# Optimization experiments

Hardware: AMD Instinct MI355X
Metric: run time of the kernel (lower is better)

## Reference

```python
import jax, jax.numpy as jnp
import numpy as np

M0, M1 = 16, 8          # scalar / vector multiplicities (16x0e + 8x1o)
NB = 16                  # number_of_basis
RMAX = 8.0               # max_radius
N_NODES, N_EDGES = 10000, 160000
WNUM = M0*M0 + M0*M1 + M1*M1 + M1*M0  # 576, tp weight_numel


def sus(t):
    """e3nn soft_unit_step: exp(-1/t) for t>0 else 0."""
    safe = jnp.where(t > 0, t, 1.0)
    return jnp.where(t > 0, jnp.exp(-1.0 / safe), 0.0)


def setup_inputs():
    key = jax.random.key(0)
    ks = jax.random.split(key, 12)
    D = M0 + 3 * M1  # 40
    x = jax.random.normal(ks[0], (N_NODES, D), jnp.float32)
    edge_index = jax.random.randint(ks[1], (2, N_EDGES), 0, N_NODES, jnp.int32)
    edge_attr = jax.random.normal(ks[2], (N_EDGES, 4), jnp.float32)  # sh lmax=1
    node_attr = jnp.ones((N_NODES, 1), jnp.float32)
    batch = jnp.zeros((N_NODES,), jnp.int32)
    amf = jax.random.uniform(ks[3], (N_EDGES, 1), jnp.float32) * RMAX  # edge lengths
    Wq0 = jax.random.normal(ks[4], (M0, M0), jnp.float32)
    Wq1 = jax.random.normal(ks[5], (M1, M1), jnp.float32)
    Wk1 = jax.random.normal(ks[6], (NB, 16), jnp.float32)
    Wk2 = jax.random.normal(ks[7], (16, WNUM), jnp.float32)
    Wv1 = jax.random.normal(ks[8], (NB, 16), jnp.float32)
    Wv2 = jax.random.normal(ks[9], (16, WNUM), jnp.float32)
    Wd0 = jax.random.normal(ks[10], (M0, M0), jnp.float32)
    Wd1 = jax.random.normal(ks[11], (M1, M1), jnp.float32)
    return dict(x=x, edge_index=edge_index, edge_attr=edge_attr, node_attr=node_attr,
                batch=batch, additional_message_features=amf,
                Wq0=Wq0, Wq1=Wq1, Wk1=Wk1, Wk2=Wk2, Wv1=Wv1, Wv2=Wv2, Wd0=Wd0, Wd1=Wd1)


def reference(x, edge_index, edge_attr, node_attr, batch, additional_message_features,
              Wq0, Wq1, Wk1, Wk2, Wv1, Wv2, Wd0, Wd1):
    n = x.shape[0]
    src, dst = edge_index[0], edge_index[1]
    d = additional_message_features.reshape(-1)  # [E]

    # soft_one_hot_linspace(basis='smooth_finite', cutoff=True) * sqrt(NB)
    centers = jnp.linspace(0.0, RMAX, NB + 2)[1:-1]
    step = RMAX / (NB + 1)
    diff = (d[:, None] - centers) / step
    emb = (1.14136 * np.exp(2.0)) * sus(diff + 1.0) * sus(1.0 - diff) * np.sqrt(NB)  # [E,NB]
    cutoff = sus(10.0 * (1.0 - d / RMAX))  # [E]

    # split irreps: scalars [*,M0], vectors [*,M1,3]
    x0 = x[:, :M0]
    x1 = x[:, M0:].reshape(n, M1, 3)

    # q = Linear(input_irreps -> hidden_irreps): per-irrep linear, 1/sqrt(fan_in)
    q0 = (x0 @ Wq0) / np.sqrt(M0)
    q1 = jnp.einsum('nui,uw->nwi', x1, Wq1) / np.sqrt(M1)

    # radial MLPs producing per-edge tensor-product weights
    def radial(W1, W2):
        h = jax.nn.silu((emb @ W1) / np.sqrt(NB))
        return (h @ W2) / np.sqrt(16.0)  # [E, WNUM]
    wk = radial(Wk1, Wk2)
    wv = radial(Wv1, Wv2)

    xs0, xs1 = x0[src], x1[src]           # gather by edge source
    sh0, sh1 = edge_attr[:, 0], edge_attr[:, 1:4]
    dot11 = jnp.einsum('eui,ei->eu', xs1, sh1) / np.sqrt(3.0)  # 1o x 1o -> 0e CG

    def fctp(w):
        # FullyConnectedTensorProduct(input, sh, out) with per-edge weights.
        s1 = M0 * M0
        s2 = s1 + M0 * M1
        s3 = s2 + M1 * M1
        w1 = w[:, :s1].reshape(-1, M0, M0)   # 0e x 0e -> 0e
        w2 = w[:, s1:s2].reshape(-1, M0, M1) # 0e x 1o -> 1o
        w3 = w[:, s2:s3].reshape(-1, M1, M1) # 1o x 0e -> 1o
        w4 = w[:, s3:].reshape(-1, M1, M0)   # 1o x 1o -> 0e
        norm = 1.0 / np.sqrt(M0 + M1)        # path fan-in normalization
        o0 = (jnp.einsum('euw,eu->ew', w1, xs0 * sh0[:, None]) +
              jnp.einsum('euw,eu->ew', w4, dot11)) * norm            # [E,M0]
        o1 = (jnp.einsum('euw,eu,ei->ewi', w2, xs0, sh1) +
              jnp.einsum('euw,eui->ewi', w3, xs1 * sh0[:, None, None])) * norm  # [E,M1,3]
        return o0, o1

    k0, k1 = fctp(wk)
    v0, v1 = fctp(wv)

    # dot: FullyConnectedTensorProduct(hidden, hidden, '0e') with shared weights
    score = (jnp.einsum('eu,ev,uv->e', q0[dst], k0, Wd0) +
             jnp.einsum('eui,evi,uv->e', q1[dst], k1, Wd1) / np.sqrt(3.0)) / np.sqrt(M0*M0 + M1*M1)

    expv = cutoff * jnp.exp(score)                                   # [E]
    z = jax.ops.segment_sum(expv, dst, num_segments=n)               # [N]
    z = jnp.where(z == 0, 1.0, z)
    alpha = expv / z[dst]
    we = jnp.sqrt(jax.nn.relu(alpha))                                # alpha.relu().sqrt()
    v = jnp.concatenate([v0, v1.reshape(-1, 3 * M1)], axis=1)        # [E,40]
    return jax.ops.segment_sum(we[:, None] * v, dst, num_segments=n) # [N,40]
```

## Files before the change

### kernel.cpp

```cpp
#include <hip/hip_runtime.h>
#include <hip/hip_bf16.h>

#define E_CNT 160000
#define N_CNT 10000

#define INV_STEP   2.125f
#define EMB_C      33.734292f
#define INVS320    0.05590170f
#define INVS8      0.35355339f
#define INV_SQRT3  0.57735027f
#define KSCALE     0.051031036f

#define OFF_FLAG   0
#define OFF_XF     16
#define OFF_EAF    400016
#define OFF_AMFF   1040016
#define OFF_WQ0F   1200016
#define OFF_WQ1F   1200272
#define OFF_WD0F   1200336
#define OFF_WD1F   1200592
#define OFF_WK1F   1200656
#define OFF_WV1F   1200912
#define OFF_WK2F   1201168
#define OFF_WV2F   1210384
#define OFF_P      1219600
#define OFF_EXPV   1619600
#define OFF_VBUF   1779600
#define OFF_DEG    8179600
#define OFF_Z      8179600
#define OFF_DEG2   8189600
#define OFF_START  8199600
#define OFF_START2 8209601
#define OFF_CURS   8219602
#define OFF_CURS2  8229602
#define OFF_DPOS   8239602
#define OFF_ELIST2 8399602
#define OFF_G      8559632

static __device__ __forceinline__ float bf2f(__hip_bfloat16 b) { return __bfloat162float(b); }
static __device__ __forceinline__ float sanitize(float v) {
    return fminf(fmaxf(v, -1e30f), 1e30f);
}
static __device__ __forceinline__ unsigned short f2bf(float f) {
    unsigned x = __float_as_uint(f);
    unsigned r = (x + 0x7fffu + ((x >> 16) & 1u)) >> 16;
    return (unsigned short)r;
}
static __device__ __forceinline__ float bflo(unsigned u) { return __uint_as_float(u << 16); }
static __device__ __forceinline__ float bfhi(unsigned u) { return __uint_as_float(u & 0xffff0000u); }

static __device__ __forceinline__ float4 load4(const void* p, int i4, int f32)
{
    if (f32) return ((const float4*)p)[i4];
    uint2 u = ((const uint2*)p)[i4];
    float4 r;
    r.x = bflo(u.x); r.y = bfhi(u.x);
    r.z = bflo(u.y); r.w = bfhi(u.y);
    return r;
}

__global__ __launch_bounds__(256) void prep_kernel(
    const void* __restrict__ x,   const void* __restrict__ ea,  const void* __restrict__ amf,
    const void* __restrict__ Wq0, const void* __restrict__ Wq1,
    const void* __restrict__ Wk1, const void* __restrict__ Wk2,
    const void* __restrict__ Wv1, const void* __restrict__ Wv2,
    const void* __restrict__ Wd0, const void* __restrict__ Wd1,
    const int* __restrict__ ei, float* __restrict__ ws)
{
    __shared__ int sflag;
    const int tid = threadIdx.x;
    if (tid == 0) {
        const unsigned short* xb = (const unsigned short*)x;
        int cnt = 0;
        for (int k = 0; k < 256; k += 2) {
            unsigned e = (unsigned)((xb[k] >> 7) & 0xFF);
            if (e >= 141) ++cnt;
        }
        sflag = (cnt >= 8) ? 1 : 0;
        if (blockIdx.x == 0) *(int*)ws = sflag;
    }
    __syncthreads();
    const int f32 = sflag;
    const int i = blockIdx.x * 256 + tid;

    if (i < 100000) ((float4*)(ws + OFF_XF))[i] = load4(x, i, f32);
    if (i < 160000) ((float4*)(ws + OFF_EAF))[i] = load4(ea, i, f32);
    if (i < 40000)  ((float4*)(ws + OFF_AMFF))[i] = load4(amf, i, f32);
    if (i < 40000) {
#pragma unroll
        for (int k = 0; k < 4; ++k) {
            atomicAdd((int*)(ws + OFF_DEG)  + ei[E_CNT + 4 * i + k], 1);
            atomicAdd((int*)(ws + OFF_DEG2) + ei[4 * i + k], 1);
        }
    }
    if (i < 2304) {
        ((float4*)(ws + OFF_WK2F))[i] = load4(Wk2, i, f32);
        ((float4*)(ws + OFF_WV2F))[i] = load4(Wv2, i, f32);
    }
    if (i < 64) {
        ((float4*)(ws + OFF_WQ0F))[i] = load4(Wq0, i, f32);
        ((float4*)(ws + OFF_WD0F))[i] = load4(Wd0, i, f32);
        ((float4*)(ws + OFF_WK1F))[i] = load4(Wk1, i, f32);
        ((float4*)(ws + OFF_WV1F))[i] = load4(Wv1, i, f32);
    }
    if (i < 16) {
        ((float4*)(ws + OFF_WQ1F))[i] = load4(Wq1, i, f32);
        ((float4*)(ws + OFF_WD1F))[i] = load4(Wd1, i, f32);
    }
}

__global__ __launch_bounds__(512) void scan_kernel(float* __restrict__ ws)
{
    __shared__ int ssum[512];
    const int t    = threadIdx.x;
    const int half = t >> 8;
    const int lt   = t & 255;
    int* deg   = (int*)(ws + (half ? OFF_DEG2   : OFF_DEG));
    int* start = (int*)(ws + (half ? OFF_START2 : OFF_START));
    int* curs  = (int*)(ws + (half ? OFF_CURS2  : OFF_CURS));
    const int base = lt * 40;
    int s = 0;
    for (int k = 0; k < 40; ++k) {
        int idx = base + k;
        if (idx < N_CNT) s += deg[idx];
    }
    ssum[t] = s;
    __syncthreads();
    for (int off = 1; off < 256; off <<= 1) {
        int v = (lt >= off) ? ssum[t - off] : 0;
        __syncthreads();
        ssum[t] += v;
        __syncthreads();
    }
    int run = ssum[t] - s;
    for (int k = 0; k < 40; ++k) {
        int idx = base + k;
        if (idx < N_CNT) {
            start[idx] = run;
            curs[idx]  = run;
            run += deg[idx];
        }
    }
    if (lt == 255) start[N_CNT] = E_CNT;
    __syncthreads();
    for (int k = t; k < N_CNT; k += 512) ws[OFF_Z + k] = 0.f;
}

__global__ __launch_bounds__(256) void fillgp_kernel(const int* __restrict__ ei, float* __restrict__ ws)
{
    const int blk = blockIdx.x;
    const int tid = threadIdx.x;
    if (blk < 625) {
        const int e = blk * 256 + tid;
        int pd = atomicAdd((int*)(ws + OFF_CURS)  + ei[E_CNT + e], 1);
        int ps = atomicAdd((int*)(ws + OFF_CURS2) + ei[e], 1);
        ((int*)(ws + OFF_ELIST2))[ps] = e;
        ((int*)(ws + OFF_DPOS))[ps]   = pd;
        return;
    }
    if (blk >= 1875) {
        const int n = (blk - 1875) * 256 + tid;
        if (n >= N_CNT) return;
        const float* WQ0 = ws + OFF_WQ0F;
        const float* WQ1 = ws + OFF_WQ1F;
        const float* WD0 = ws + OFF_WD0F;
        const float* WD1 = ws + OFF_WD1F;
        float xs[40];
        const float4* xr = (const float4*)(ws + OFF_XF + n * 40);
#pragma unroll
        for (int k = 0; k < 10; ++k) {
            float4 f = xr[k];
            xs[4 * k + 0] = f.x; xs[4 * k + 1] = f.y; xs[4 * k + 2] = f.z; xs[4 * k + 3] = f.w;
        }
        float q0[16];
#pragma unroll
        for (int w = 0; w < 16; ++w) {
            float s = 0.f;
#pragma unroll
            for (int u = 0; u < 16; ++u) s = fmaf(xs[u], WQ0[u * 16 + w], s);
            q0[w] = s * 0.25f;
        }
        float* pn = ws + OFF_P + n * 40;
#pragma unroll
        for (int v = 0; v < 16; ++v) {
            float s = 0.f;
#pragma unroll
            for (int w = 0; w < 16; ++w) s = fmaf(q0[w], WD0[w * 16 + v], s);
            pn[v] = sanitize(s * INVS320);
        }
        float q1[24];
#pragma unroll
        for (int w = 0; w < 8; ++w) {
            float s0 = 0.f, s1 = 0.f, s2 = 0.f;
#pragma unroll
            for (int u = 0; u < 8; ++u) {
                float wq = WQ1[u * 8 + w];
                s0 = fmaf(xs[16 + u * 3 + 0], wq, s0);
                s1 = fmaf(xs[16 + u * 3 + 1], wq, s1);
                s2 = fmaf(xs[16 + u * 3 + 2], wq, s2);
            }
            q1[w * 3 + 0] = s0 * INVS8;
            q1[w * 3 + 1] = s1 * INVS8;
            q1[w * 3 + 2] = s2 * INVS8;
        }
#pragma unroll
        for (int v = 0; v < 8; ++v) {
            float s0 = 0.f, s1 = 0.f, s2 = 0.f;
#pragma unroll
            for (int w = 0; w < 8; ++w) {
                float wd = WD1[w * 8 + v];
                s0 = fmaf(q1[w * 3 + 0], wd, s0);
                s1 = fmaf(q1[w * 3 + 1], wd, s1);
                s2 = fmaf(q1[w * 3 + 2], wd, s2);
            }
            const float sc = INVS320 * INV_SQRT3;
            pn[16 + v * 3 + 0] = sanitize(s0 * sc);
            pn[16 + v * 3 + 1] = sanitize(s1 * sc);
            pn[16 + v * 3 + 2] = sanitize(s2 * sc);
        }
        return;
    }
    const int t = (blk - 625) * 256 + tid;
    const int p   = t / 160000;
    const int rem = t - p * 160000;
    const int c   = rem / 10000;
    const int n   = rem - c * 10000;

    const float* W2 = ws + (p ? OFF_WV2F : OFF_WK2F) + c * 576;
    float x0[16], x1[24];
    {
        const float4* xr = (const float4*)(ws + OFF_XF + n * 40);
        float xs[40];
#pragma unroll
        for (int k = 0; k < 10; ++k) {
            float4 f = xr[k];
            xs[4 * k + 0] = f.x; xs[4 * k + 1] = f.y; xs[4 * k + 2] = f.z; xs[4 * k + 3] = f.w;
        }
#pragma unroll
        for (int u = 0; u < 16; ++u) x0[u] = xs[u];
#pragma unroll
        for (int u = 0; u < 24; ++u) x1[u] = xs[16 + u];
    }

    float out[96];
#pragma unroll
    for (int w = 0; w < 16; ++w) {
        float s = 0.f;
#pragma unroll
        for (int u = 0; u < 16; ++u) s = fmaf(W2[u * 16 + w], x0[u], s);
        out[w] = s;
    }
#pragma unroll
    for (int w = 0; w < 8; ++w) {
        float s = 0.f;
#pragma unroll
        for (int u = 0; u < 16; ++u) s = fmaf(W2[256 + u * 8 + w], x0[u], s);
        out[16 + w] = s;
    }
#pragma unroll
    for (int w = 0; w < 8; ++w) {
        float s0 = 0.f, s1 = 0.f, s2 = 0.f;
#pragma unroll
        for (int u = 0; u < 8; ++u) {
            float wv = W2[384 + u * 8 + w];
            s0 = fmaf(wv, x1[u * 3 + 0], s0);
            s1 = fmaf(wv, x1[u * 3 + 1], s1);
            s2 = fmaf(wv, x1[u * 3 + 2], s2);
        }
        out[24 + w * 3 + 0] = s0;
        out[24 + w * 3 + 1] = s1;
        out[24 + w * 3 + 2] = s2;
    }
#pragma unroll
    for (int w = 0; w < 16; ++w) {
        float s0 = 0.f, s1 = 0.f, s2 = 0.f;
#pragma unroll
        for (int u = 0; u < 8; ++u) {
            float wv = W2[448 + u * 16 + w];
            s0 = fmaf(wv, x1[u * 3 + 0], s0);
            s1 = fmaf(wv, x1[u * 3 + 1], s1);
            s2 = fmaf(wv, x1[u * 3 + 2], s2);
        }
        out[48 + w * 3 + 0] = s0 * INV_SQRT3;
        out[48 + w * 3 + 1] = s1 * INV_SQRT3;
        out[48 + w * 3 + 2] = s2 * INV_SQRT3;
    }

    uint4 ov[12];
    unsigned* ou = (unsigned*)ov;
#pragma unroll
    for (int k = 0; k < 48; ++k)
        ou[k] = (unsigned)f2bf(out[2 * k]) | ((unsigned)f2bf(out[2 * k + 1]) << 16);
    uint4* dp = (uint4*)((unsigned short*)(ws + OFF_G) + ((size_t)n * 2 + p) * 1536 + c * 96);
#pragma unroll
    for (int q = 0; q < 12; ++q) dp[q] = ov[q];
}

static __device__ __forceinline__ void load48(unsigned (&ub)[48], const uint4* __restrict__ rp)
{
#pragma unroll
    for (int q = 0; q < 12; ++q) {
        uint4 v = rp[q];
        ub[4 * q + 0] = v.x; ub[4 * q + 1] = v.y;
        ub[4 * q + 2] = v.z; ub[4 * q + 3] = v.w;
    }
}

static __device__ __forceinline__ void accum48(const unsigned (&ub)[48], float hc, float sh0,
    float s1x, float s1y, float s1z,
    float (&o0)[16], float (&o1)[24], float (&t2a)[8])
{
    const float hs = hc * sh0;
#define GVAL(k) (((k) & 1) ? bfhi(ub[(k) >> 1]) : bflo(ub[(k) >> 1]))
#pragma unroll
    for (int w = 0; w < 16; ++w) o0[w] = fmaf(hs, GVAL(w), o0[w]);
#pragma unroll
    for (int w = 0; w < 8; ++w) t2a[w] = fmaf(hc, GVAL(16 + w), t2a[w]);
#pragma unroll
    for (int w = 0; w < 8; ++w) {
        o1[w * 3 + 0] = fmaf(hs, GVAL(24 + w * 3 + 0), o1[w * 3 + 0]);
        o1[w * 3 + 1] = fmaf(hs, GVAL(24 + w * 3 + 1), o1[w * 3 + 1]);
        o1[w * 3 + 2] = fmaf(hs, GVAL(24 + w * 3 + 2), o1[w * 3 + 2]);
    }
#pragma unroll
    for (int w = 0; w < 16; ++w) {
        float g = GVAL(48 + w * 3 + 0) * s1x;
        g = fmaf(GVAL(48 + w * 3 + 1), s1y, g);
        g = fmaf(GVAL(48 + w * 3 + 2), s1z, g);
        o0[w] = fmaf(hc, g, o0[w]);
    }
#undef GVAL
}

__global__ __launch_bounds__(256, 2) void edge_kernel(
    const int* __restrict__ ei, float* __restrict__ ws)
{
    __shared__ float h_s[16 * 256];
    const int tid  = threadIdx.x;
    const int pass = tid >> 7;
    const int lane = tid & 127;
    const int b  = blockIdx.x;
    const int lb = (b < 1248) ? ((b & 7) * 156 + (b >> 3)) : b;
    const int sidx = lb * 128 + lane;
    const int e    = ((const int*)(ws + OFF_ELIST2))[sidx];
    const int dpos = ((const int*)(ws + OFF_DPOS))[sidx];
    const int src  = ei[e];
    const int dst  = ei[E_CNT + e];

    const float d   = ws[OFF_AMFF + e];
    const float dsv = d * INV_STEP;
    float emb[16];
#pragma unroll
    for (int bb = 0; bb < 16; ++bb) {
        float t1 = dsv - (float)bb;
        float t2 = (float)(bb + 2) - dsv;
        float v = 0.f;
        if (t1 > 0.f && t2 > 0.f) v = EMB_C * expf(-1.f / t1 - 1.f / t2);
        emb[bb] = v;
    }

    const float* W1 = ws + (pass ? OFF_WV1F : OFF_WK1F);
#pragma unroll 1
    for (int j = 0; j < 16; ++j) {
        float s = 0.f;
#pragma unroll
        for (int bb = 0; bb < 16; ++bb) s = fmaf(emb[bb], W1[bb * 16 + j], s);
        s *= 0.25f;
        h_s[j * 256 + tid] = s / (1.f + expf(-s));
    }

    const float4 eav = ((const float4*)(ws + OFF_EAF))[e];
    const float sh0 = eav.x, s1x = eav.y, s1y = eav.z, s1z = eav.w;

    float o0[16], o1[24], t2a[8];
#pragma unroll
    for (int i = 0; i < 16; ++i) o0[i] = 0.f;
#pragma unroll
    for (int i = 0; i < 24; ++i) o1[i] = 0.f;
#pragma unroll
    for (int i = 0; i < 8; ++i) t2a[i] = 0.f;

    const uint4* Gp = (const uint4*)((const unsigned short*)(ws + OFF_G)
                                     + ((size_t)src * 2 + pass) * 1536);

    unsigned A[48], B[48];
    load48(A, Gp);
#pragma unroll 1
    for (int c = 0; c < 16; c += 2) {
        load48(B, Gp + (c + 1) * 12);
        accum48(A, h_s[c * 256 + tid], sh0, s1x, s1y, s1z, o0, o1, t2a);
        if (c + 2 < 16) load48(A, Gp + (c + 2) * 12);
        accum48(B, h_s[(c + 1) * 256 + tid], sh0, s1x, s1y, s1z, o0, o1, t2a);
    }

#pragma unroll
    for (int w = 0; w < 8; ++w) {
        o1[w * 3 + 0] = fmaf(t2a[w], s1x, o1[w * 3 + 0]);
        o1[w * 3 + 1] = fmaf(t2a[w], s1y, o1[w * 3 + 1]);
        o1[w * 3 + 2] = fmaf(t2a[w], s1z, o1[w * 3 + 2]);
    }

    if (pass == 0) {
        const float* pd = ws + OFF_P + dst * 40;
        float sc = 0.f;
#pragma unroll
        for (int j = 0; j < 16; ++j) sc = fmaf(o0[j], pd[j], sc);
#pragma unroll
        for (int j = 0; j < 24; ++j) sc = fmaf(o1[j], pd[16 + j], sc);
        sc = fminf(fmaxf(sc * KSCALE, -60.f), 60.f);
        float ct = 10.f * (1.f - d * 0.125f);
        float cutoff = (ct > 0.f) ? expf(-1.f / ct) : 0.f;
        float ev = fmaxf(cutoff * expf(sc), 0.f);
        ws[OFF_EXPV + dpos] = ev;
        atomicAdd(ws + OFF_Z + dst, ev);
    } else {
        float* vr = ws + OFF_VBUF + (size_t)dpos * 40;
#pragma unroll
        for (int j = 0; j < 16; ++j) vr[j] = sanitize(o0[j] * KSCALE);
#pragma unroll
        for (int j = 0; j < 24; ++j) vr[16 + j] = sanitize(o1[j] * KSCALE);
    }
}

__global__ __launch_bounds__(256) void gather_kernel(
    const float* __restrict__ ws, void* __restrict__ out)
{
    const int i = blockIdx.x * 256 + threadIdx.x;
    if (i >= N_CNT * 40) return;
    const int n = i / 40;
    const int f = i - n * 40;
    const int* start = (const int*)(ws + OFF_START);
    const float* expv = ws + OFF_EXPV;
    const float* Vbuf = ws + OFF_VBUF;
    const int s = start[n], t = start[n + 1];

    float zz = ws[OFF_Z + n];
    const float rz = (zz > 0.f) ? 1.f / zz : 1.f;

    float acc = 0.f;
    for (int j = s; j < t; ++j) {
        const float we = sqrtf(fmaxf(expv[j] * rz, 0.f));
        acc = fmaf(we, Vbuf[(size_t)j * 40 + f], acc);
    }
    acc = sanitize(acc);
    const int f32 = *(const int*)ws;
    if (f32) ((float*)out)[i] = acc;
    else     ((__hip_bfloat16*)out)[i] = __float2bfloat16(acc);
}

extern "C" void kernel_launch(void* const* d_in, const int* in_sizes, int n_in,
                              void* d_out, int out_size, void* d_ws, size_t ws_size,
                              hipStream_t stream)
{
    (void)in_sizes; (void)n_in; (void)out_size; (void)ws_size;
    const void* x   = d_in[0];
    const int*  ei  = (const int*)d_in[1];
    const void* ea  = d_in[2];
    const void* amf = d_in[5];
    const void* Wq0 = d_in[6];
    const void* Wq1 = d_in[7];
    const void* Wk1 = d_in[8];
    const void* Wk2 = d_in[9];
    const void* Wv1 = d_in[10];
    const void* Wv2 = d_in[11];
    const void* Wd0 = d_in[12];
    const void* Wd1 = d_in[13];

    float* ws = (float*)d_ws;

    hipMemsetAsync(ws + OFF_DEG, 0, 20000 * sizeof(int), stream);
    prep_kernel<<<625, 256, 0, stream>>>(x, ea, amf, Wq0, Wq1, Wk1, Wk2, Wv1, Wv2, Wd0, Wd1, ei, ws);
    scan_kernel<<<1, 512, 0, stream>>>(ws);
    fillgp_kernel<<<1915, 256, 0, stream>>>(ei, ws);
    edge_kernel<<<1250, 256, 0, stream>>>(ei, ws);
    gather_kernel<<<(N_CNT * 40 + 255) / 256, 256, 0, stream>>>(ws, d_out);
}
```

Measured before the change: 310.1 us.

## Build G and P directly from inputs in prep, shrink edge blocks, vectorize gather

Moves the per-node G and P construction out of the fill kernel into the prep kernel. They now read x and the weights straight from the inputs through a templated converter, which removes the staged float copies of x and the weight matrices. The fill kernel shrinks to the CSR scatter only. The edge kernel moves to 128-thread blocks with 4 blocks per SIMD bound and a remapped block order, and the gather kernel handles four features per thread with float4 loads and stores. The trade-off is that the G and P builders now convert from bf16 inside their loops and read input weights from global memory directly.

Measured after the change: 661.1 us. 113% more time.

```diff
diff --git a/kernel.cpp b/kernel.cpp
--- a/kernel.cpp
+++ b/kernel.cpp
@@ -15,14 +15,8 @@
 #define OFF_XF     16
 #define OFF_EAF    400016
 #define OFF_AMFF   1040016
-#define OFF_WQ0F   1200016
-#define OFF_WQ1F   1200272
-#define OFF_WD0F   1200336
-#define OFF_WD1F   1200592
 #define OFF_WK1F   1200656
 #define OFF_WV1F   1200912
-#define OFF_WK2F   1201168
-#define OFF_WV2F   1210384
 #define OFF_P      1219600
 #define OFF_EXPV   1619600
 #define OFF_VBUF   1779600
@@ -38,6 +32,8 @@
 #define OFF_G      8559632
 
 static __device__ __forceinline__ float bf2f(__hip_bfloat16 b) { return __bfloat162float(b); }
+static __device__ __forceinline__ float cvt(float v) { return v; }
+static __device__ __forceinline__ float cvt(__hip_bfloat16 v) { return bf2f(v); }
 static __device__ __forceinline__ float sanitize(float v) {
     return fminf(fmaxf(v, -1e30f), 1e30f);
 }
@@ -59,7 +55,128 @@
     return r;
 }
 
-__global__ __launch_bounds__(256) void prep_kernel(
+template <typename T>
+static __device__ __forceinline__ void build_G(
+    const T* __restrict__ x, const T* __restrict__ W2b, int n, int p, int c, float* __restrict__ ws)
+{
+    float xs[40];
+#pragma unroll
+    for (int u = 0; u < 40; ++u) xs[u] = cvt(x[n * 40 + u]);
+    const T* W2 = W2b + c * 576;
+    const float* x0 = xs;
+    const float* x1 = xs + 16;
+
+    float out[96];
+#pragma unroll
+    for (int w = 0; w < 16; ++w) {
+        float s = 0.f;
+#pragma unroll
+        for (int u = 0; u < 16; ++u) s = fmaf(cvt(W2[u * 16 + w]), x0[u], s);
+        out[w] = s;
+    }
+#pragma unroll
+    for (int w = 0; w < 8; ++w) {
+        float s = 0.f;
+#pragma unroll
+        for (int u = 0; u < 16; ++u) s = fmaf(cvt(W2[256 + u * 8 + w]), x0[u], s);
+        out[16 + w] = s;
+    }
+#pragma unroll
+    for (int w = 0; w < 8; ++w) {
+        float s0 = 0.f, s1 = 0.f, s2 = 0.f;
+#pragma unroll
+        for (int u = 0; u < 8; ++u) {
+            float wv = cvt(W2[384 + u * 8 + w]);
+            s0 = fmaf(wv, x1[u * 3 + 0], s0);
+            s1 = fmaf(wv, x1[u * 3 + 1], s1);
+            s2 = fmaf(wv, x1[u * 3 + 2], s2);
+        }
+        out[24 + w * 3 + 0] = s0;
+        out[24 + w * 3 + 1] = s1;
+        out[24 + w * 3 + 2] = s2;
+    }
+#pragma unroll
+    for (int w = 0; w < 16; ++w) {
+        float s0 = 0.f, s1 = 0.f, s2 = 0.f;
+#pragma unroll
+        for (int u = 0; u < 8; ++u) {
+            float wv = cvt(W2[448 + u * 16 + w]);
+            s0 = fmaf(wv, x1[u * 3 + 0], s0);
+            s1 = fmaf(wv, x1[u * 3 + 1], s1);
+            s2 = fmaf(wv, x1[u * 3 + 2], s2);
+        }
+        out[48 + w * 3 + 0] = s0 * INV_SQRT3;
+        out[48 + w * 3 + 1] = s1 * INV_SQRT3;
+        out[48 + w * 3 + 2] = s2 * INV_SQRT3;
+    }
+
+    uint4 ov[12];
+    unsigned* ou = (unsigned*)ov;
+#pragma unroll
+    for (int k = 0; k < 48; ++k)
+        ou[k] = (unsigned)f2bf(out[2 * k]) | ((unsigned)f2bf(out[2 * k + 1]) << 16);
+    uint4* dp = (uint4*)((unsigned short*)(ws + OFF_G) + ((size_t)n * 2 + p) * 1536 + c * 96);
+#pragma unroll
+    for (int q = 0; q < 12; ++q) dp[q] = ov[q];
+}
+
+template <typename T>
+static __device__ __forceinline__ void build_P(
+    const T* __restrict__ x, const T* __restrict__ Wq0, const T* __restrict__ Wq1,
+    const T* __restrict__ Wd0, const T* __restrict__ Wd1, int n, float* __restrict__ ws)
+{
+    float xs[40];
+#pragma unroll
+    for (int u = 0; u < 40; ++u) xs[u] = cvt(x[n * 40 + u]);
+    float q0[16];
+#pragma unroll
+    for (int w = 0; w < 16; ++w) {
+        float s = 0.f;
+#pragma unroll
+        for (int u = 0; u < 16; ++u) s = fmaf(xs[u], cvt(Wq0[u * 16 + w]), s);
+        q0[w] = s * 0.25f;
+    }
+    float* pn = ws + OFF_P + n * 40;
+#pragma unroll
+    for (int v = 0; v < 16; ++v) {
+        float s = 0.f;
+#pragma unroll
+        for (int w = 0; w < 16; ++w) s = fmaf(q0[w], cvt(Wd0[w * 16 + v]), s);
+        pn[v] = sanitize(s * INVS320);
+    }
+    float q1[24];
+#pragma unroll
+    for (int w = 0; w < 8; ++w) {
+        float s0 = 0.f, s1 = 0.f, s2 = 0.f;
+#pragma unroll
+        for (int u = 0; u < 8; ++u) {
+            float wq = cvt(Wq1[u * 8 + w]);
+            s0 = fmaf(xs[16 + u * 3 + 0], wq, s0);
+            s1 = fmaf(xs[16 + u * 3 + 1], wq, s1);
+            s2 = fmaf(xs[16 + u * 3 + 2], wq, s2);
+        }
+        q1[w * 3 + 0] = s0 * INVS8;
+        q1[w * 3 + 1] = s1 * INVS8;
+        q1[w * 3 + 2] = s2 * INVS8;
+    }
+#pragma unroll
+    for (int v = 0; v < 8; ++v) {
+        float s0 = 0.f, s1 = 0.f, s2 = 0.f;
+#pragma unroll
+        for (int w = 0; w < 8; ++w) {
+            float wd = cvt(Wd1[w * 8 + v]);
+            s0 = fmaf(q1[w * 3 + 0], wd, s0);
+            s1 = fmaf(q1[w * 3 + 1], wd, s1);
+            s2 = fmaf(q1[w * 3 + 2], wd, s2);
+        }
+        const float sc = INVS320 * INV_SQRT3;
+        pn[16 + v * 3 + 0] = sanitize(s0 * sc);
+        pn[16 + v * 3 + 1] = sanitize(s1 * sc);
+        pn[16 + v * 3 + 2] = sanitize(s2 * sc);
+    }
+}
+
+__global__ __launch_bounds__(256) void prepgp_kernel(
     const void* __restrict__ x,   const void* __restrict__ ea,  const void* __restrict__ amf,
     const void* __restrict__ Wq0, const void* __restrict__ Wq1,
     const void* __restrict__ Wk1, const void* __restrict__ Wk2,
@@ -69,6 +186,7 @@
 {
     __shared__ int sflag;
     const int tid = threadIdx.x;
+    const int blk = blockIdx.x;
     if (tid == 0) {
         const unsigned short* xb = (const unsigned short*)x;
         int cnt = 0;
@@ -77,35 +195,47 @@
             if (e >= 141) ++cnt;
         }
         sflag = (cnt >= 8) ? 1 : 0;
-        if (blockIdx.x == 0) *(int*)ws = sflag;
+        if (blk == 0) *(int*)ws = sflag;
     }
     __syncthreads();
     const int f32 = sflag;
-    const int i = blockIdx.x * 256 + tid;
-
-    if (i < 100000) ((float4*)(ws + OFF_XF))[i] = load4(x, i, f32);
-    if (i < 160000) ((float4*)(ws + OFF_EAF))[i] = load4(ea, i, f32);
-    if (i < 40000)  ((float4*)(ws + OFF_AMFF))[i] = load4(amf, i, f32);
-    if (i < 40000) {
-#pragma unroll
-        for (int k = 0; k < 4; ++k) {
-            atomicAdd((int*)(ws + OFF_DEG)  + ei[E_CNT + 4 * i + k], 1);
-            atomicAdd((int*)(ws + OFF_DEG2) + ei[4 * i + k], 1);
-        }
-    }
-    if (i < 2304) {
-        ((float4*)(ws + OFF_WK2F))[i] = load4(Wk2, i, f32);
-        ((float4*)(ws + OFF_WV2F))[i] = load4(Wv2, i, f32);
-    }
-    if (i < 64) {
-        ((float4*)(ws + OFF_WQ0F))[i] = load4(Wq0, i, f32);
-        ((float4*)(ws + OFF_WD0F))[i] = load4(Wd0, i, f32);
-        ((float4*)(ws + OFF_WK1F))[i] = load4(Wk1, i, f32);
-        ((float4*)(ws + OFF_WV1F))[i] = load4(Wv1, i, f32);
-    }
-    if (i < 16) {
-        ((float4*)(ws + OFF_WQ1F))[i] = load4(Wq1, i, f32);
-        ((float4*)(ws + OFF_WD1F))[i] = load4(Wd1, i, f32);
+
+    if (blk < 625) {
+        const int i = blk * 256 + tid;
+        if (i < 160000) ((float4*)(ws + OFF_EAF))[i] = load4(ea, i, f32);
+        if (i < 40000) {
+            ((float4*)(ws + OFF_AMFF))[i] = load4(amf, i, f32);
+#pragma unroll
+            for (int k = 0; k < 4; ++k) {
+                atomicAdd((int*)(ws + OFF_DEG)  + ei[E_CNT + 4 * i + k], 1);
+                atomicAdd((int*)(ws + OFF_DEG2) + ei[4 * i + k], 1);
+            }
+        }
+        if (i < 64) {
+            ((float4*)(ws + OFF_WK1F))[i] = load4(Wk1, i, f32);
+            ((float4*)(ws + OFF_WV1F))[i] = load4(Wv1, i, f32);
+        }
+        return;
+    }
+    if (blk < 1875) {
+        const int t = (blk - 625) * 256 + tid;
+        const int p   = t / 160000;
+        const int rem = t - p * 160000;
+        const int c   = rem / 10000;
+        const int n   = rem - c * 10000;
+        const void* W2b = p ? Wv2 : Wk2;
+        if (f32) build_G((const float*)x, (const float*)W2b, n, p, c, ws);
+        else     build_G((const __hip_bfloat16*)x, (const __hip_bfloat16*)W2b, n, p, c, ws);
+        return;
+    }
+    {
+        const int n = (blk - 1875) * 256 + tid;
+        if (n >= N_CNT) return;
+        if (f32) build_P((const float*)x, (const float*)Wq0, (const float*)Wq1,
+                         (const float*)Wd0, (const float*)Wd1, n, ws);
+        else     build_P((const __hip_bfloat16*)x, (const __hip_bfloat16*)Wq0,
+                         (const __hip_bfloat16*)Wq1, (const __hip_bfloat16*)Wd0,
+                         (const __hip_bfloat16*)Wd1, n, ws);
     }
 }
 
@@ -146,154 +276,13 @@
     for (int k = t; k < N_CNT; k += 512) ws[OFF_Z + k] = 0.f;
 }
 
-__global__ __launch_bounds__(256) void fillgp_kernel(const int* __restrict__ ei, float* __restrict__ ws)
-{
-    const int blk = blockIdx.x;
-    const int tid = threadIdx.x;
-    if (blk < 625) {
-        const int e = blk * 256 + tid;
-        int pd = atomicAdd((int*)(ws + OFF_CURS)  + ei[E_CNT + e], 1);
-        int ps = atomicAdd((int*)(ws + OFF_CURS2) + ei[e], 1);
-        ((int*)(ws + OFF_ELIST2))[ps] = e;
-        ((int*)(ws + OFF_DPOS))[ps]   = pd;
-        return;
-    }
-    if (blk >= 1875) {
-        const int n = (blk - 1875) * 256 + tid;
-        if (n >= N_CNT) return;
-        const float* WQ0 = ws + OFF_WQ0F;
-        const float* WQ1 = ws + OFF_WQ1F;
-        const float* WD0 = ws + OFF_WD0F;
-        const float* WD1 = ws + OFF_WD1F;
-        float xs[40];
-        const float4* xr = (const float4*)(ws + OFF_XF + n * 40);
-#pragma unroll
-        for (int k = 0; k < 10; ++k) {
-            float4 f = xr[k];
-            xs[4 * k + 0] = f.x; xs[4 * k + 1] = f.y; xs[4 * k + 2] = f.z; xs[4 * k + 3] = f.w;
-        }
-        float q0[16];
-#pragma unroll
-        for (int w = 0; w < 16; ++w) {
-            float s = 0.f;
-#pragma unroll
-            for (int u = 0; u < 16; ++u) s = fmaf(xs[u], WQ0[u * 16 + w], s);
-            q0[w] = s * 0.25f;
-        }
-        float* pn = ws + OFF_P + n * 40;
-#pragma unroll
-        for (int v = 0; v < 16; ++v) {
-            float s = 0.f;
-#pragma unroll
-            for (int w = 0; w < 16; ++w) s = fmaf(q0[w], WD0[w * 16 + v], s);
-            pn[v] = sanitize(s * INVS320);
-        }
-        float q1[24];
-#pragma unroll
-        for (int w = 0; w < 8; ++w) {
-            float s0 = 0.f, s1 = 0.f, s2 = 0.f;
-#pragma unroll
-            for (int u = 0; u < 8; ++u) {
-                float wq = WQ1[u * 8 + w];
-                s0 = fmaf(xs[16 + u * 3 + 0], wq, s0);
-                s1 = fmaf(xs[16 + u * 3 + 1], wq, s1);
-                s2 = fmaf(xs[16 + u * 3 + 2], wq, s2);
-            }
-            q1[w * 3 + 0] = s0 * INVS8;
-            q1[w * 3 + 1] = s1 * INVS8;
-            q1[w * 3 + 2] = s2 * INVS8;
-        }
-#pragma unroll
-        for (int v = 0; v < 8; ++v) {
-            float s0 = 0.f, s1 = 0.f, s2 = 0.f;
-#pragma unroll
-            for (int w = 0; w < 8; ++w) {
-                float wd = WD1[w * 8 + v];
-                s0 = fmaf(q1[w * 3 + 0], wd, s0);
-                s1 = fmaf(q1[w * 3 + 1], wd, s1);
-                s2 = fmaf(q1[w * 3 + 2], wd, s2);
-            }
-            const float sc = INVS320 * INV_SQRT3;
-            pn[16 + v * 3 + 0] = sanitize(s0 * sc);
-            pn[16 + v * 3 + 1] = sanitize(s1 * sc);
-            pn[16 + v * 3 + 2] = sanitize(s2 * sc);
-        }
-        return;
-    }
-    const int t = (blk - 625) * 256 + tid;
-    const int p   = t / 160000;
-    const int rem = t - p * 160000;
-    const int c   = rem / 10000;
-    const int n   = rem - c * 10000;
-
-    const float* W2 = ws + (p ? OFF_WV2F : OFF_WK2F) + c * 576;
-    float x0[16], x1[24];
-    {
-        const float4* xr = (const float4*)(ws + OFF_XF + n * 40);
-        float xs[40];
-#pragma unroll
-        for (int k = 0; k < 10; ++k) {
-            float4 f = xr[k];
-            xs[4 * k + 0] = f.x; xs[4 * k + 1] = f.y; xs[4 * k + 2] = f.z; xs[4 * k + 3] = f.w;
-        }
-#pragma unroll
-        for (int u = 0; u < 16; ++u) x0[u] = xs[u];
-#pragma unroll
-        for (int u = 0; u < 24; ++u) x1[u] = xs[16 + u];
-    }
-
-    float out[96];
-#pragma unroll
-    for (int w = 0; w < 16; ++w) {
-        float s = 0.f;
-#pragma unroll
-        for (int u = 0; u < 16; ++u) s = fmaf(W2[u * 16 + w], x0[u], s);
-        out[w] = s;
-    }
-#pragma unroll
-    for (int w = 0; w < 8; ++w) {
-        float s = 0.f;
-#pragma unroll
-        for (int u = 0; u < 16; ++u) s = fmaf(W2[256 + u * 8 + w], x0[u], s);
-        out[16 + w] = s;
-    }
-#pragma unroll
-    for (int w = 0; w < 8; ++w) {
-        float s0 = 0.f, s1 = 0.f, s2 = 0.f;
-#pragma unroll
-        for (int u = 0; u < 8; ++u) {
-            float wv = W2[384 + u * 8 + w];
-            s0 = fmaf(wv, x1[u * 3 + 0], s0);
-            s1 = fmaf(wv, x1[u * 3 + 1], s1);
-            s2 = fmaf(wv, x1[u * 3 + 2], s2);
-        }
-        out[24 + w * 3 + 0] = s0;
-        out[24 + w * 3 + 1] = s1;
-        out[24 + w * 3 + 2] = s2;
-    }
-#pragma unroll
-    for (int w = 0; w < 16; ++w) {
-        float s0 = 0.f, s1 = 0.f, s2 = 0.f;
-#pragma unroll
-        for (int u = 0; u < 8; ++u) {
-            float wv = W2[448 + u * 16 + w];
-            s0 = fmaf(wv, x1[u * 3 + 0], s0);
-            s1 = fmaf(wv, x1[u * 3 + 1], s1);
-            s2 = fmaf(wv, x1[u * 3 + 2], s2);
-        }
-        out[48 + w * 3 + 0] = s0 * INV_SQRT3;
-        out[48 + w * 3 + 1] = s1 * INV_SQRT3;
-        out[48 + w * 3 + 2] = s2 * INV_SQRT3;
-    }
-
-    uint4 ov[12];
-    unsigned* ou = (unsigned*)ov;
-#pragma unroll
-    for (int k = 0; k < 48; ++k)
-        ou[k] = (unsigned)f2bf(out[2 * k]) | ((unsigned)f2bf(out[2 * k + 1]) << 16);
-    uint4* dp = (uint4*)((unsigned short*)(ws + OFF_G) + ((size_t)n * 2 + p) * 1536 + c * 96);
-#pragma unroll
-    for (int q = 0; q < 12; ++q) dp[q] = ov[q];
+__global__ __launch_bounds__(256) void fill_kernel(const int* __restrict__ ei, float* __restrict__ ws)
+{
+    const int e = blockIdx.x * 256 + threadIdx.x;
+    int pd = atomicAdd((int*)(ws + OFF_CURS)  + ei[E_CNT + e], 1);
+    int ps = atomicAdd((int*)(ws + OFF_CURS2) + ei[e], 1);
+    ((int*)(ws + OFF_ELIST2))[ps] = e;
+    ((int*)(ws + OFF_DPOS))[ps]   = pd;
 }
 
 static __device__ __forceinline__ void load48(unsigned (&ub)[48], const uint4* __restrict__ rp)
@@ -332,16 +321,16 @@
 #undef GVAL
 }
 
-__global__ __launch_bounds__(256, 2) void edge_kernel(
+__global__ __launch_bounds__(128, 4) void edge_kernel(
     const int* __restrict__ ei, float* __restrict__ ws)
 {
-    __shared__ float h_s[16 * 256];
+    __shared__ float h_s[16 * 128];
     const int tid  = threadIdx.x;
-    const int pass = tid >> 7;
-    const int lane = tid & 127;
+    const int pass = tid >> 6;
+    const int lane = tid & 63;
     const int b  = blockIdx.x;
-    const int lb = (b < 1248) ? ((b & 7) * 156 + (b >> 3)) : b;
-    const int sidx = lb * 128 + lane;
+    const int lb = (b < 2496) ? ((b & 7) * 312 + (b >> 3)) : b;
+    const int sidx = lb * 64 + lane;
     const int e    = ((const int*)(ws + OFF_ELIST2))[sidx];
     const int dpos = ((const int*)(ws + OFF_DPOS))[sidx];
     const int src  = ei[e];
@@ -366,7 +355,7 @@
 #pragma unroll
         for (int bb = 0; bb < 16; ++bb) s = fmaf(emb[bb], W1[bb * 16 + j], s);
         s *= 0.25f;
-        h_s[j * 256 + tid] = s / (1.f + expf(-s));
+        h_s[j * 128 + tid] = s / (1.f + expf(-s));
     }
 
     const float4 eav = ((const float4*)(ws + OFF_EAF))[e];
@@ -388,9 +377,9 @@
 #pragma unroll 1
     for (int c = 0; c < 16; c += 2) {
         load48(B, Gp + (c + 1) * 12);
-        accum48(A, h_s[c * 256 + tid], sh0, s1x, s1y, s1z, o0, o1, t2a);
+        accum48(A, h_s[c * 128 + tid], sh0, s1x, s1y, s1z, o0, o1, t2a);
         if (c + 2 < 16) load48(A, Gp + (c + 2) * 12);
-        accum48(B, h_s[(c + 1) * 256 + tid], sh0, s1x, s1y, s1z, o0, o1, t2a);
+        accum48(B, h_s[(c + 1) * 128 + tid], sh0, s1x, s1y, s1z, o0, o1, t2a);
     }
 
 #pragma unroll
@@ -426,26 +415,35 @@
     const float* __restrict__ ws, void* __restrict__ out)
 {
     const int i = blockIdx.x * 256 + threadIdx.x;
-    if (i >= N_CNT * 40) return;
-    const int n = i / 40;
-    const int f = i - n * 40;
+    if (i >= N_CNT * 10) return;
+    const int n = i / 10;
+    const int q = i - n * 10;
     const int* start = (const int*)(ws + OFF_START);
     const float* expv = ws + OFF_EXPV;
-    const float* Vbuf = ws + OFF_VBUF;
+    const float4* Vbuf4 = (const float4*)(ws + OFF_VBUF);
     const int s = start[n], t = start[n + 1];
 
     float zz = ws[OFF_Z + n];
     const float rz = (zz > 0.f) ? 1.f / zz : 1.f;
 
-    float acc = 0.f;
+    float ax = 0.f, ay = 0.f, az = 0.f, aw = 0.f;
     for (int j = s; j < t; ++j) {
         const float we = sqrtf(fmaxf(expv[j] * rz, 0.f));
-        acc = fmaf(we, Vbuf[(size_t)j * 40 + f], acc);
-    }
-    acc = sanitize(acc);
+        float4 v = Vbuf4[(size_t)j * 10 + q];
+        ax = fmaf(we, v.x, ax); ay = fmaf(we, v.y, ay);
+        az = fmaf(we, v.z, az); aw = fmaf(we, v.w, aw);
+    }
+    ax = sanitize(ax); ay = sanitize(ay); az = sanitize(az); aw = sanitize(aw);
     const int f32 = *(const int*)ws;
-    if (f32) ((float*)out)[i] = acc;
-    else     ((__hip_bfloat16*)out)[i] = __float2bfloat16(acc);
+    if (f32) {
+        float4 o; o.x = ax; o.y = ay; o.z = az; o.w = aw;
+        ((float4*)out)[(size_t)n * 10 + q] = o;
+    } else {
+        uint2 o;
+        o.x = (unsigned)f2bf(ax) | ((unsigned)f2bf(ay) << 16);
+        o.y = (unsigned)f2bf(az) | ((unsigned)f2bf(aw) << 16);
+        ((uint2*)out)[(size_t)n * 10 + q] = o;
+    }
 }
 
 extern "C" void kernel_launch(void* const* d_in, const int* in_sizes, int n_in,
@@ -469,9 +467,9 @@
     float* ws = (float*)d_ws;
 
     hipMemsetAsync(ws + OFF_DEG, 0, 20000 * sizeof(int), stream);
-    prep_kernel<<<625, 256, 0, stream>>>(x, ea, amf, Wq0, Wq1, Wk1, Wk2, Wv1, Wv2, Wd0, Wd1, ei, ws);
+    prepgp_kernel<<<1915, 256, 0, stream>>>(x, ea, amf, Wq0, Wq1, Wk1, Wk2, Wv1, Wv2, Wd0, Wd1, ei, ws);
     scan_kernel<<<1, 512, 0, stream>>>(ws);
-    fillgp_kernel<<<1915, 256, 0, stream>>>(ei, ws);
-    edge_kernel<<<1250, 256, 0, stream>>>(ei, ws);
-    gather_kernel<<<(N_CNT * 40 + 255) / 256, 256, 0, stream>>>(ws, d_out);
-}
+    fill_kernel<<<625, 256, 0, stream>>>(ei, ws);
+    edge_kernel<<<2500, 128, 0, stream>>>(ei, ws);
+    gather_kernel<<<(N_CNT * 10 + 255) / 256, 256, 0, stream>>>(ws, d_out);
+}
```
